# Kernel tuning notes

Hardware: AMD Instinct MI355X
Metric: run time of the kernel (lower is better)

## Reference

```python
import jax, jax.numpy as jnp
import numpy as np

HIDDEN = 4096


def setup_inputs() -> dict:
    key = jax.random.key(0)
    k1, k2 = jax.random.split(key)
    hidden_states = jax.random.normal(k1, (8, 2048, HIDDEN), dtype=jnp.float32)
    # gate_proj ~ N(0, 0.02^2), shape (2*hidden, hidden)
    gate_proj = 0.02 * jax.random.normal(k2, (2 * HIDDEN, HIDDEN), dtype=jnp.float32)
    return {"hidden_states": hidden_states, "gate_proj": gate_proj, "world_size": 8}


def reference(hidden_states, gate_proj, world_size):
    h = gate_proj.shape[1]
    view = hidden_states.reshape(-1, h)                 # [N, h]
    mm = jnp.einsum("nh,oh->no", view, gate_proj)      # [N, 2h]  (x @ W.T)
    n, o = mm.shape
    # reduce-scatter over dim 0 with world_size ranks: sum the per-rank chunks
    out = mm.reshape(world_size, n // world_size, o).sum(axis=0)  # [N/W, 2h]
    return out
```

## Files before the change

kernel.cpp:

```cpp
#include <hip/hip_runtime.h>
#include <hip/hip_bf16.h>


#define HID   4096
#define SEQ   2048
#define WORLD 8
#define OUTD  8192

typedef __bf16 bf16x8 __attribute__((ext_vector_type(8)));
typedef short  s16x8  __attribute__((ext_vector_type(8)));
typedef float  f32x4  __attribute__((ext_vector_type(4)));

typedef const __attribute__((address_space(1))) void* gas1_ptr;
typedef __attribute__((address_space(3))) void*       las3_ptr;

static __device__ __forceinline__ unsigned short f2bf(float f) {
    union { float f; unsigned u; } v; v.f = f;
    unsigned u = v.u;
    u += 0x7fffu + ((u >> 16) & 1u);
    return (unsigned short)(u >> 16);
}

__global__ void reduce_x_kernel(const float* __restrict__ hs,
                                unsigned short* __restrict__ xb) {
    const int total4 = SEQ * HID / 4;
    const float4* h4 = (const float4*)hs;
    ushort4* o4 = (ushort4*)xb;
    for (int i = blockIdx.x * blockDim.x + threadIdx.x; i < total4;
         i += gridDim.x * blockDim.x) {
        float4 s = h4[i];
        #pragma unroll
        for (int w = 1; w < WORLD; ++w) {
            float4 t = h4[i + w * total4];
            s.x += t.x; s.y += t.y; s.z += t.z; s.w += t.w;
        }
        ushort4 o;
        o.x = f2bf(s.x); o.y = f2bf(s.y); o.z = f2bf(s.z); o.w = f2bf(s.w);
        o4[i] = o;
    }
}

__global__ void convert_w_kernel(const float* __restrict__ w,
                                 unsigned short* __restrict__ wb) {
    const int total4 = OUTD * HID / 4;
    const float4* w4 = (const float4*)w;
    ushort4* o4 = (ushort4*)wb;
    for (int i = blockIdx.x * blockDim.x + threadIdx.x; i < total4;
         i += gridDim.x * blockDim.x) {
        float4 s = w4[i];
        ushort4 o;
        o.x = f2bf(s.x); o.y = f2bf(s.y); o.z = f2bf(s.z); o.w = f2bf(s.w);
        o4[i] = o;
    }
}


#define BM 128
#define BN 128
#define BK 64
#define KSTEPS (HID / BK)

__global__ __launch_bounds__(256, 2)
void gemm_bt_kernel(const unsigned short* __restrict__ A,
                    const unsigned short* __restrict__ B,
                    float* __restrict__ C) {
    __shared__ __align__(16) unsigned short lsA[BM * BK];
    __shared__ __align__(16) unsigned short lsB[BN * BK];

    const int tid  = threadIdx.x;
    const int lane = tid & 63;
    const int wave = tid >> 6;

    const int nbn = OUTD / BN;
    const int bm  = blockIdx.x / nbn;
    const int bn  = blockIdx.x % nbn;

    const int st_subrow = lane >> 3;
    const int st_slot   = lane & 7;
    const int scol      = (st_slot ^ st_subrow) * 8;

    const unsigned short* aPtr =
        A + (long)(bm * BM + wave * 8 + st_subrow) * HID + scol;
    const unsigned short* bPtr =
        B + (long)(bn * BN + wave * 8 + st_subrow) * HID + scol;
    const int ldsWave = wave * 8 * BK;

    const int wr = (wave >> 1) * 64;
    const int wc = (wave & 1) * 64;
    const int fr = lane & 15;
    const int fq = lane >> 4;
    const int axor = fr & 7;

    f32x4 acc[4][4] = {};

    for (int kt = 0; kt < KSTEPS; ++kt) {
        const unsigned short* ap = aPtr + kt * BK;
        const unsigned short* bp = bPtr + kt * BK;
        #pragma unroll
        for (int r = 0; r < 4; ++r) {
            __builtin_amdgcn_global_load_lds(
                (gas1_ptr)(ap + (long)r * 32 * HID),
                (las3_ptr)(&lsA[ldsWave + r * 32 * BK]), 16, 0, 0);
            __builtin_amdgcn_global_load_lds(
                (gas1_ptr)(bp + (long)r * 32 * HID),
                (las3_ptr)(&lsB[ldsWave + r * 32 * BK]), 16, 0, 0);
        }
        __syncthreads();

        bf16x8 va[4][2], vb[4][2];
        #pragma unroll
        for (int m = 0; m < 4; ++m) {
            const int row = wr + m * 16 + fr;
            #pragma unroll
            for (int s = 0; s < 2; ++s) {
                const int kslot = s * 4 + fq;
                const int off = row * BK + ((kslot ^ axor) * 8);
                va[m][s] = __builtin_bit_cast(bf16x8, *(const s16x8*)&lsA[off]);
            }
        }
        #pragma unroll
        for (int n = 0; n < 4; ++n) {
            const int row = wc + n * 16 + fr;
            #pragma unroll
            for (int s = 0; s < 2; ++s) {
                const int kslot = s * 4 + fq;
                const int off = row * BK + ((kslot ^ axor) * 8);
                vb[n][s] = __builtin_bit_cast(bf16x8, *(const s16x8*)&lsB[off]);
            }
        }
        #pragma unroll
        for (int s = 0; s < 2; ++s)
            #pragma unroll
            for (int m = 0; m < 4; ++m)
                #pragma unroll
                for (int n = 0; n < 4; ++n)
                    acc[m][n] = __builtin_amdgcn_mfma_f32_16x16x32_bf16(
                        va[m][s], vb[n][s], acc[m][n], 0, 0, 0);

        __syncthreads();
    }

    const long crow0 = (long)bm * BM + wr + fq * 4;
    const long ccol0 = (long)bn * BN + wc + fr;
    #pragma unroll
    for (int m = 0; m < 4; ++m)
        #pragma unroll
        for (int n = 0; n < 4; ++n)
            #pragma unroll
            for (int j = 0; j < 4; ++j)
                C[(crow0 + m * 16 + j) * OUTD + ccol0 + n * 16] = acc[m][n][j];
}

extern "C" void kernel_launch(void* const* d_in, const int* in_sizes, int n_in,
                              void* d_out, int out_size, void* d_ws, size_t ws_size,
                              hipStream_t stream) {
    const float* hs = (const float*)d_in[0];
    const float* w  = (const float*)d_in[1];
    float* out = (float*)d_out;

    unsigned short* xb = (unsigned short*)d_ws;
    unsigned short* wb = xb + (size_t)SEQ * HID;

    hipLaunchKernelGGL(reduce_x_kernel, dim3(2048), dim3(256), 0, stream, hs, xb);
    hipLaunchKernelGGL(convert_w_kernel, dim3(4096), dim3(256), 0, stream, w, wb);
    hipLaunchKernelGGL(gemm_bt_kernel, dim3((SEQ / BM) * (OUTD / BN)), dim3(256),
                       0, stream, xb, wb, out);
}
```

Baseline: 235.4 us.

## Use 256x256 tiles with double-buffered LDS and interleaved load/MFMA schedule

```diff
diff --git a/kernel.cpp b/kernel.cpp
--- a/kernel.cpp
+++ b/kernel.cpp
@@ -55,95 +55,157 @@
 }
 
 
-#define BM 128
-#define BN 128
+#define BM 256
+#define BN 256
 #define BK 64
 #define KSTEPS (HID / BK)
 
-__global__ __launch_bounds__(256, 2)
+__global__ __launch_bounds__(512, 2)
 void gemm_bt_kernel(const unsigned short* __restrict__ A,
                     const unsigned short* __restrict__ B,
                     float* __restrict__ C) {
-    __shared__ __align__(16) unsigned short lsA[BM * BK];
-    __shared__ __align__(16) unsigned short lsB[BN * BK];
+    __shared__ __align__(16) unsigned short lsA[2][BM * BK];
+    __shared__ __align__(16) unsigned short lsB[2][BN * BK];
 
     const int tid  = threadIdx.x;
     const int lane = tid & 63;
     const int wave = tid >> 6;
-
-    const int nbn = OUTD / BN;
-    const int bm  = blockIdx.x / nbn;
-    const int bn  = blockIdx.x % nbn;
-
-    const int st_subrow = lane >> 3;
-    const int st_slot   = lane & 7;
-    const int scol      = (st_slot ^ st_subrow) * 8;
-
-    const unsigned short* aPtr =
-        A + (long)(bm * BM + wave * 8 + st_subrow) * HID + scol;
-    const unsigned short* bPtr =
-        B + (long)(bn * BN + wave * 8 + st_subrow) * HID + scol;
-    const int ldsWave = wave * 8 * BK;
-
-    const int wr = (wave >> 1) * 64;
-    const int wc = (wave & 1) * 64;
-    const int fr = lane & 15;
-    const int fq = lane >> 4;
-    const int axor = fr & 7;
-
-    f32x4 acc[4][4] = {};
+    const int wm   = wave >> 2;
+    const int wn   = wave & 3;
+
+    const int bid    = blockIdx.x;
+    const int tileid = (bid & 7) * 32 + (bid >> 3);
+    const int bm = tileid >> 5;
+    const int bn = tileid & 31;
+
+    const int subrow = lane >> 3;
+    const int slot   = lane & 7;
+    const int scol   = (slot ^ subrow) * 8;
+    const unsigned short* aBase =
+        A + (size_t)(bm * BM + wave * 8 + subrow) * HID + scol;
+    const unsigned short* bBase =
+        B + (size_t)(bn * BN + wave * 8 + subrow) * HID + scol;
+    const int ldsW = wave * 8 * BK;
+
+#define ST_A(buf, ktv, l) __builtin_amdgcn_global_load_lds(                     \
+        (gas1_ptr)(aBase + (size_t)(ktv) * BK + (size_t)(l) * 64 * HID),        \
+        (las3_ptr)(&lsA[buf][(l) * 64 * BK + ldsW]), 16, 0, 0)
+#define ST_B(buf, ktv, l) __builtin_amdgcn_global_load_lds(                     \
+        (gas1_ptr)(bBase + (size_t)(ktv) * BK + (size_t)(l) * 64 * HID),        \
+        (las3_ptr)(&lsB[buf][(l) * 64 * BK + ldsW]), 16, 0, 0)
+
+    const int fr    = lane & 15;
+    const int fq    = lane >> 4;
+    const int axor  = fr & 7;
+    const int koff0 = ((0 + fq) ^ axor) * 8;
+    const int koff1 = ((4 + fq) ^ axor) * 8;
+    const int aRowB = (wm * 128 + fr) * BK;
+    const int bRowB = (wn * 64 + fr) * BK;
+
+#define RD_A(dst, p, mm, koff) dst = __builtin_bit_cast(bf16x8,                 \
+        *(const s16x8*)&lsA[p][aRowB + (mm) * 16 * BK + (koff)])
+#define RD_B(dst, p, nn, koff) dst = __builtin_bit_cast(bf16x8,                 \
+        *(const s16x8*)&lsB[p][bRowB + (nn) * 16 * BK + (koff)])
+
+#define BARRIER() __builtin_amdgcn_s_barrier()
+#define LGKM0()   asm volatile("s_waitcnt lgkmcnt(0)" ::: "memory")
+#define VMC4()    asm volatile("s_waitcnt vmcnt(4)" ::: "memory")
+#define VMC0()    asm volatile("s_waitcnt vmcnt(0)" ::: "memory")
+#define PRIO1()   __builtin_amdgcn_s_setprio(1)
+#define PRIO0()   __builtin_amdgcn_s_setprio(0)
+
+    f32x4 acc[8][4] = {};
+    bf16x8 va[4][2], vb[4][2];
+
+    ST_A(0, 0, 0); ST_A(0, 0, 1); ST_A(0, 0, 2); ST_A(0, 0, 3);
+    ST_B(0, 0, 0); ST_B(0, 0, 1); ST_B(0, 0, 2); ST_B(0, 0, 3);
+    ST_A(1, 1, 0); ST_A(1, 1, 1); ST_A(1, 1, 2); ST_A(1, 1, 3);
+    VMC4();
+    BARRIER();
 
     for (int kt = 0; kt < KSTEPS; ++kt) {
-        const unsigned short* ap = aPtr + kt * BK;
-        const unsigned short* bp = bPtr + kt * BK;
-        #pragma unroll
-        for (int r = 0; r < 4; ++r) {
-            __builtin_amdgcn_global_load_lds(
-                (gas1_ptr)(ap + (long)r * 32 * HID),
-                (las3_ptr)(&lsA[ldsWave + r * 32 * BK]), 16, 0, 0);
-            __builtin_amdgcn_global_load_lds(
-                (gas1_ptr)(bp + (long)r * 32 * HID),
-                (las3_ptr)(&lsB[ldsWave + r * 32 * BK]), 16, 0, 0);
-        }
-        __syncthreads();
-
-        bf16x8 va[4][2], vb[4][2];
-        #pragma unroll
-        for (int m = 0; m < 4; ++m) {
-            const int row = wr + m * 16 + fr;
-            #pragma unroll
-            for (int s = 0; s < 2; ++s) {
-                const int kslot = s * 4 + fq;
-                const int off = row * BK + ((kslot ^ axor) * 8);
-                va[m][s] = __builtin_bit_cast(bf16x8, *(const s16x8*)&lsA[off]);
-            }
-        }
-        #pragma unroll
-        for (int n = 0; n < 4; ++n) {
-            const int row = wc + n * 16 + fr;
-            #pragma unroll
-            for (int s = 0; s < 2; ++s) {
-                const int kslot = s * 4 + fq;
-                const int off = row * BK + ((kslot ^ axor) * 8);
-                vb[n][s] = __builtin_bit_cast(bf16x8, *(const s16x8*)&lsB[off]);
-            }
-        }
-        #pragma unroll
-        for (int s = 0; s < 2; ++s)
-            #pragma unroll
-            for (int m = 0; m < 4; ++m)
-                #pragma unroll
-                for (int n = 0; n < 4; ++n)
+        const int p = kt & 1;
+        const int q = p ^ 1;
+        const bool s1 = (kt + 1 < KSTEPS);
+        const bool s2 = (kt + 2 < KSTEPS);
+
+        RD_A(va[0][0], p, 0, koff0); RD_A(va[0][1], p, 0, koff1);
+        RD_A(va[1][0], p, 1, koff0); RD_A(va[1][1], p, 1, koff1);
+        RD_A(va[2][0], p, 2, koff0); RD_A(va[2][1], p, 2, koff1);
+        RD_A(va[3][0], p, 3, koff0); RD_A(va[3][1], p, 3, koff1);
+        RD_B(vb[0][0], p, 0, koff0); RD_B(vb[0][1], p, 0, koff1);
+        RD_B(vb[1][0], p, 1, koff0); RD_B(vb[1][1], p, 1, koff1);
+        if (s1) { ST_B(q, kt + 1, 0); ST_B(q, kt + 1, 1); }
+        BARRIER();
+        LGKM0();
+        PRIO1();
+        #pragma unroll
+        for (int s = 0; s < 2; ++s)
+            #pragma unroll
+            for (int m = 0; m < 4; ++m)
+                #pragma unroll
+                for (int n = 0; n < 2; ++n)
                     acc[m][n] = __builtin_amdgcn_mfma_f32_16x16x32_bf16(
                         va[m][s], vb[n][s], acc[m][n], 0, 0, 0);
-
-        __syncthreads();
+        PRIO0();
+        BARRIER();
+
+        RD_B(vb[2][0], p, 2, koff0); RD_B(vb[2][1], p, 2, koff1);
+        RD_B(vb[3][0], p, 3, koff0); RD_B(vb[3][1], p, 3, koff1);
+        if (s1) { ST_B(q, kt + 1, 2); ST_B(q, kt + 1, 3); }
+        BARRIER();
+        LGKM0();
+        PRIO1();
+        #pragma unroll
+        for (int s = 0; s < 2; ++s)
+            #pragma unroll
+            for (int m = 0; m < 4; ++m)
+                #pragma unroll
+                for (int n = 0; n < 2; ++n)
+                    acc[m][2 + n] = __builtin_amdgcn_mfma_f32_16x16x32_bf16(
+                        va[m][s], vb[2 + n][s], acc[m][2 + n], 0, 0, 0);
+        PRIO0();
+        BARRIER();
+
+        RD_A(va[0][0], p, 4, koff0); RD_A(va[0][1], p, 4, koff1);
+        RD_A(va[1][0], p, 5, koff0); RD_A(va[1][1], p, 5, koff1);
+        RD_A(va[2][0], p, 6, koff0); RD_A(va[2][1], p, 6, koff1);
+        RD_A(va[3][0], p, 7, koff0); RD_A(va[3][1], p, 7, koff1);
+        BARRIER();
+        LGKM0();
+        PRIO1();
+        #pragma unroll
+        for (int s = 0; s < 2; ++s)
+            #pragma unroll
+            for (int m = 0; m < 4; ++m)
+                #pragma unroll
+                for (int n = 0; n < 2; ++n)
+                    acc[4 + m][n] = __builtin_amdgcn_mfma_f32_16x16x32_bf16(
+                        va[m][s], vb[n][s], acc[4 + m][n], 0, 0, 0);
+        PRIO0();
+        BARRIER();
+
+        if (s2) { ST_A(p, kt + 2, 0); ST_A(p, kt + 2, 1);
+                  ST_A(p, kt + 2, 2); ST_A(p, kt + 2, 3); }
+        BARRIER();
+        PRIO1();
+        #pragma unroll
+        for (int s = 0; s < 2; ++s)
+            #pragma unroll
+            for (int m = 0; m < 4; ++m)
+                #pragma unroll
+                for (int n = 0; n < 2; ++n)
+                    acc[4 + m][2 + n] = __builtin_amdgcn_mfma_f32_16x16x32_bf16(
+                        va[m][s], vb[2 + n][s], acc[4 + m][2 + n], 0, 0, 0);
+        PRIO0();
+        if (s2) { VMC4(); } else { VMC0(); }
+        BARRIER();
     }
 
-    const long crow0 = (long)bm * BM + wr + fq * 4;
-    const long ccol0 = (long)bn * BN + wc + fr;
+    const long crow0 = (long)bm * BM + wm * 128 + fq * 4;
+    const long ccol0 = (long)bn * BN + wn * 64 + fr;
     #pragma unroll
-    for (int m = 0; m < 4; ++m)
+    for (int m = 0; m < 8; ++m)
         #pragma unroll
         for (int n = 0; n < 4; ++n)
             #pragma unroll
@@ -163,6 +225,6 @@
 
     hipLaunchKernelGGL(reduce_x_kernel, dim3(2048), dim3(256), 0, stream, hs, xb);
     hipLaunchKernelGGL(convert_w_kernel, dim3(4096), dim3(256), 0, stream, w, wb);
-    hipLaunchKernelGGL(gemm_bt_kernel, dim3((SEQ / BM) * (OUTD / BN)), dim3(256),
+    hipLaunchKernelGGL(gemm_bt_kernel, dim3((SEQ / BM) * (OUTD / BN)), dim3(512),
                        0, stream, xb, wb, out);
 }
```

New measurement: 242.0 us. +2.8%, slower.
